# Performance work log

Measured on AMD Instinct MI355X. Metric: run time of the kernel, lower is better.

## Reference

```python
import jax, jax.numpy as jnp
import numpy as np

B, S, D_MODEL, H = 2, 2048, 1024, 16
HD = D_MODEL // H  # 64


def rotate_half(x):
    # pairs (x_even, x_odd) -> (-x_odd, x_even), interleaved back
    x1 = x[..., ::2]
    x2 = x[..., 1::2]
    return jnp.stack([-x2, x1], axis=-1).reshape(x.shape)


def rope_sin_cos(seq_len, head_dim):
    pos = jnp.arange(seq_len, dtype=jnp.float32)
    dim = jnp.arange(head_dim, dtype=jnp.float32)
    theta = 10000.0 ** (-2.0 * jnp.floor(dim / 2.0) / head_dim)
    angles = pos[:, None] * theta[None, :]  # [S, HD]
    return jnp.sin(angles), jnp.cos(angles)


def setup_inputs():
    key = jax.random.key(0)
    ks = jax.random.split(key, 6)
    w_scale = 1.0 / np.sqrt(D_MODEL)
    x = jax.random.normal(ks[0], (B, S, D_MODEL), jnp.float32)
    # causal mask: 1.0 where attention is disallowed (j > i)
    mask = (1.0 - jnp.tril(jnp.ones((S, S), jnp.float32)))[None, None, :, :]
    wq = jax.random.normal(ks[1], (D_MODEL, D_MODEL), jnp.float32) * w_scale
    wk = jax.random.normal(ks[2], (D_MODEL, D_MODEL), jnp.float32) * w_scale
    wv = jax.random.normal(ks[3], (D_MODEL, D_MODEL), jnp.float32) * w_scale
    wo = jax.random.normal(ks[4], (D_MODEL, D_MODEL), jnp.float32) * w_scale
    zeros = jnp.zeros((D_MODEL,), jnp.float32)
    return dict(x=x, mask=mask, wq=wq, bq=zeros, wk=wk, bk=zeros,
                wv=wv, bv=zeros, wo=wo, bo=zeros)


def reference(x, mask, wq, bq, wk, bk, wv, bv, wo, bo):
    b, s, _ = x.shape

    def split_heads(t):  # [B,S,D] -> [B,H,S,HD]
        return t.reshape(b, s, H, HD).transpose(0, 2, 1, 3)

    q = split_heads(x @ wq + bq)
    k = split_heads(x @ wk + bk)
    v = split_heads(x @ wv + bv)

    sin, cos = rope_sin_cos(s, HD)
    sin = sin[None, None, :, :]
    cos = cos[None, None, :, :]
    q = q * cos + rotate_half(q) * sin
    k = k * cos + rotate_half(k) * sin

    logits = jnp.einsum('bhqd,bhkd->bhqk', q, k) / jnp.sqrt(jnp.float32(HD))
    logits = logits + mask * (-1e9)
    attn = jax.nn.softmax(logits, axis=-1)
    out = jnp.einsum('bhqk,bhkd->bhqd', attn, v)  # [B,H,S,HD]
    out = out.transpose(0, 2, 1, 3).reshape(b, s, D_MODEL)
    return out @ wo + bo
```

## Files before the change

kernel.cpp:

```cpp
#include <hip/hip_runtime.h>
#include <hip/hip_bf16.h>


#define S_ 2048
#define DM 1024
#define HD 64

typedef __attribute__((ext_vector_type(8))) short short8;
typedef __attribute__((ext_vector_type(4))) float floatx4;

__device__ __forceinline__ unsigned short f2b(float x) {
  union { __hip_bfloat16 h; unsigned short u; } cv;
  cv.h = __float2bfloat16(x);
  return cv.u;
}

__device__ __forceinline__ void gload_lds16(const unsigned short* g, unsigned short* l) {
  typedef const __attribute__((address_space(1))) unsigned int* gp_t;
  typedef __attribute__((address_space(3))) unsigned int* lp_t;
  __builtin_amdgcn_global_load_lds((gp_t)(const void*)g, (lp_t)(void*)l, 16, 0, 0);
}

__global__ void prep_kernel(const float* __restrict__ x,
                            const float* __restrict__ w0, const float* __restrict__ w1,
                            const float* __restrict__ w2, const float* __restrict__ w3,
                            unsigned short* __restrict__ xc,
                            unsigned short* __restrict__ wt,
                            float2* __restrict__ rope) {
  const int bid = blockIdx.x;
  if (bid < 4096) {
    int i = (bid * 256 + threadIdx.x) * 4;
    float4 v = *(const float4*)(x + i);
    ushort4 o;
    o.x = f2b(v.x); o.y = f2b(v.y); o.z = f2b(v.z); o.w = f2b(v.w);
    *(ushort4*)(xc + i) = o;
  } else if (bid < 8192) {
    __shared__ float tile[32][33];
    const int rem = bid - 4096;
    const int z = rem >> 10;
    const int bx = (rem & 1023) & 31;
    const int by = (rem & 1023) >> 5;
    const float* W = (z == 0) ? w0 : (z == 1) ? w1 : (z == 2) ? w2 : w3;
    unsigned short* Wt = wt + (size_t)z * DM * DM;
    const int tx = threadIdx.x & 31;
    const int ty = threadIdx.x >> 5;
    const int k0 = bx * 32;
    const int c0 = by * 32;
#pragma unroll
    for (int i = 0; i < 4; ++i)
      tile[ty + i * 8][tx] = W[(size_t)(k0 + ty + i * 8) * DM + c0 + tx];
    __syncthreads();
#pragma unroll
    for (int i = 0; i < 4; ++i)
      Wt[(size_t)(c0 + ty + i * 8) * DM + k0 + tx] = f2b(tile[tx][ty + i * 8]);
  } else {
    int i = (bid - 8192) * 256 + threadIdx.x;
    int s = i >> 5, d2 = i & 31;
    float th = expf(-(float)d2 * (9.210340371976184f / 32.0f));
    float sn, cs;
    sincosf((float)s * th, &sn, &cs);
    rope[i] = make_float2(cs, sn);
  }
}

__global__ __launch_bounds__(256, 3) void gemm_qkv(
    const unsigned short* __restrict__ A, const unsigned short* __restrict__ Wt,
    const float* __restrict__ bq, const float* __restrict__ bk,
    const float* __restrict__ bv, const float2* __restrict__ rope,
    unsigned short* __restrict__ QKV) {
  __shared__ __attribute__((aligned(16))) unsigned short As[128 * 64];
  __shared__ __attribute__((aligned(16))) unsigned short Bs[128 * 64];
  const int r0 = blockIdx.x * 128;
  const int c0 = blockIdx.y * 128;
  const int t = threadIdx.x;
  const int lane = t & 63;
  const int wv = t >> 6;
  const int wr = (wv >> 1) * 64;
  const int wc = (wv & 1) * 64;
  const int lr = lane & 15;
  const int lg = lane >> 4;

  const int srow = wv * 32 + (lane >> 3);
  const int sseg = ((lane & 7) ^ (lane >> 3)) * 8;
  const unsigned short* Ag = A + (size_t)(r0 + srow) * DM + sseg;
  const unsigned short* Bg = Wt + (size_t)(c0 + srow) * DM + sseg;
  unsigned short* lA = &As[wv * 32 * 64];
  unsigned short* lB = &Bs[wv * 32 * 64];

  floatx4 acc[4][4] = {};
  const int fswz = (lr & 7) << 4;

  for (int k0 = 0; k0 < DM; k0 += 64) {
#pragma unroll
    for (int j = 0; j < 4; ++j) {
      gload_lds16(Ag + k0 + j * 8 * DM, lA + j * 8 * 64);
      gload_lds16(Bg + k0 + j * 8 * DM, lB + j * 8 * 64);
    }
    __syncthreads();
#pragma unroll
    for (int kk = 0; kk < 2; ++kk) {
      short8 af[4], bf[4];
#pragma unroll
      for (int m = 0; m < 4; ++m)
        af[m] = *(const short8*)((char*)As + (wr + m * 16 + lr) * 128 +
                                 ((kk * 64 + lg * 16) ^ fswz));
#pragma unroll
      for (int n = 0; n < 4; ++n)
        bf[n] = *(const short8*)((char*)Bs + (wc + n * 16 + lr) * 128 +
                                 ((kk * 64 + lg * 16) ^ fswz));
#pragma unroll
      for (int m = 0; m < 4; ++m)
#pragma unroll
        for (int n = 0; n < 4; ++n)
          acc[m][n] = __builtin_amdgcn_mfma_f32_16x16x32_bf16(af[m], bf[n], acc[m][n], 0, 0, 0);
    }
    __syncthreads();
  }

  const int mat = blockIdx.y >> 3;
  const float* bias = (mat == 0) ? bq : (mat == 1) ? bk : bv;
  const int rbase = r0 + wr + lg * 4;
  const int cbase = c0 + wc + lr;
#pragma unroll
  for (int n = 0; n < 4; ++n) {
    const int c = cbase + n * 16;
    const int cc = c & (DM - 1);
    const float bvv = bias[cc];
    const int d = c & 63;
    const int h = cc >> 6;
#pragma unroll
    for (int m = 0; m < 4; ++m) {
#pragma unroll
      for (int i = 0; i < 4; ++i) {
        const int r = rbase + m * 16 + i;
        const int s = r & (S_ - 1);
        const int b = r >> 11;
        float v = acc[m][n][i] + bvv;
        float pv = __shfl_xor(v, 1);
        if (mat < 2) {
          float2 cssn = rope[s * 32 + (d >> 1)];
          v = (d & 1) ? fmaf(v, cssn.x, pv * cssn.y) : fmaf(v, cssn.x, -pv * cssn.y);
          if (mat == 0) v *= 0.18033688011112042f;
        }
        QKV[((size_t)((mat << 5) | (b << 4) | h) * S_ + s) * HD + d] = f2b(v);
      }
    }
  }
}

__global__ __launch_bounds__(256, 3) void gemm_out(
    const unsigned short* __restrict__ A, const unsigned short* __restrict__ Wt,
    const float* __restrict__ bias, float* __restrict__ out) {
  __shared__ __attribute__((aligned(16))) unsigned short As[128 * 64];
  __shared__ __attribute__((aligned(16))) unsigned short Bs[128 * 64];
  const int r0 = blockIdx.x * 128;
  const int c0 = blockIdx.y * 128;
  const int t = threadIdx.x;
  const int lane = t & 63;
  const int wv = t >> 6;
  const int wr = (wv >> 1) * 64;
  const int wc = (wv & 1) * 64;
  const int lr = lane & 15;
  const int lg = lane >> 4;

  const int srow = wv * 32 + (lane >> 3);
  const int sseg = ((lane & 7) ^ (lane >> 3)) * 8;
  const unsigned short* Ag = A + (size_t)(r0 + srow) * DM + sseg;
  const unsigned short* Bg = Wt + (size_t)(c0 + srow) * DM + sseg;
  unsigned short* lA = &As[wv * 32 * 64];
  unsigned short* lB = &Bs[wv * 32 * 64];

  floatx4 acc[4][4] = {};
  const int fswz = (lr & 7) << 4;

  for (int k0 = 0; k0 < DM; k0 += 64) {
#pragma unroll
    for (int j = 0; j < 4; ++j) {
      gload_lds16(Ag + k0 + j * 8 * DM, lA + j * 8 * 64);
      gload_lds16(Bg + k0 + j * 8 * DM, lB + j * 8 * 64);
    }
    __syncthreads();
#pragma unroll
    for (int kk = 0; kk < 2; ++kk) {
      short8 af[4], bf[4];
#pragma unroll
      for (int m = 0; m < 4; ++m)
        af[m] = *(const short8*)((char*)As + (wr + m * 16 + lr) * 128 +
                                 ((kk * 64 + lg * 16) ^ fswz));
#pragma unroll
      for (int n = 0; n < 4; ++n)
        bf[n] = *(const short8*)((char*)Bs + (wc + n * 16 + lr) * 128 +
                                 ((kk * 64 + lg * 16) ^ fswz));
#pragma unroll
      for (int m = 0; m < 4; ++m)
#pragma unroll
        for (int n = 0; n < 4; ++n)
          acc[m][n] = __builtin_amdgcn_mfma_f32_16x16x32_bf16(af[m], bf[n], acc[m][n], 0, 0, 0);
    }
    __syncthreads();
  }

  const int rbase = r0 + wr + lg * 4;
  const int cbase = c0 + wc + lr;
#pragma unroll
  for (int n = 0; n < 4; ++n) {
    const int c = cbase + n * 16;
    const float bvv = bias[c];
#pragma unroll
    for (int m = 0; m < 4; ++m) {
#pragma unroll
      for (int i = 0; i < 4; ++i) {
        const int r = rbase + m * 16 + i;
        out[(size_t)r * DM + c] = acc[m][n][i] + bvv;
      }
    }
  }
}

__global__ __launch_bounds__(256, 4) void attn_kernel(
    const unsigned short* __restrict__ Q, const unsigned short* __restrict__ K,
    const unsigned short* __restrict__ V, unsigned short* __restrict__ AttnC) {
  __shared__ __attribute__((aligned(16))) unsigned short Ks[2][64 * 64];
  __shared__ __attribute__((aligned(16))) unsigned short Vs[2][64 * 64];
  __shared__ __attribute__((aligned(16))) unsigned short Ps[4][16 * 64];

  const int bh = blockIdx.x;
  const int y = (int)blockIdx.y;
  const int ya = y >> 3, yb = y & 7;
  const int qt = (ya & 1) ? (8 * ya + 7 - yb) : (8 * ya + yb);
  const int tid = threadIdx.x;
  const int w = tid >> 6;
  const int l = tid & 63;
  const int lg = l >> 4;
  const int lr = l & 15;
  const size_t base = (size_t)bh * S_ * HD;
  const int qin = w * 16 + lr;

  short8 qf[2];
  {
    const unsigned short* Qrow =
        Q + base + (size_t)(qt * 64 + w * 16 + lr) * HD + lg * 8;
    qf[0] = *(const short8*)(Qrow);
    qf[1] = *(const short8*)(Qrow + 32);
  }

  floatx4 o[4] = {};
  float m = -1e30f, lsum = 0.f;

  const int krow = tid >> 3;
  const int kseg = tid & 7;
  const int oct = tid >> 5;
  const int kp = tid & 31;

  int4 kr0, kr1; short8 va, vb;
  {
    const unsigned short* Kg = K + base;
    const unsigned short* Vg = V + base;
    kr0 = *(const int4*)(Kg + krow * 64 + kseg * 8);
    kr1 = *(const int4*)(Kg + (krow + 32) * 64 + kseg * 8);
    va = *(const short8*)(Vg + (2 * kp) * 64 + oct * 8);
    vb = *(const short8*)(Vg + (2 * kp + 1) * 64 + oct * 8);
  }

  char* const Pw = (char*)Ps[w];
  const int pswz = (lr & 7) << 4;

  for (int t = 0; t <= qt; ++t) {
    const int cur = t & 1;
    {
      char* Kb = (char*)Ks[cur];
      *(int4*)(Kb + krow * 128 + ((kseg * 16) ^ ((krow & 7) << 4))) = kr0;
      *(int4*)(Kb + (krow + 32) * 128 + ((kseg * 16) ^ ((krow & 7) << 4))) = kr1;
      char* Vb = (char*)Vs[cur];
#pragma unroll
      for (int j = 0; j < 8; ++j) {
        int d = oct * 8 + j;
        unsigned int pk = (unsigned int)(unsigned short)va[j] |
                          ((unsigned int)(unsigned short)vb[j] << 16);
        *(unsigned int*)(Vb + d * 128 + ((4 * kp) ^ (j << 4))) = pk;
      }
    }
    if (t < qt) {
      const unsigned short* Kg = K + base + (size_t)(t + 1) * 64 * HD;
      const unsigned short* Vg = V + base + (size_t)(t + 1) * 64 * HD;
      kr0 = *(const int4*)(Kg + krow * 64 + kseg * 8);
      kr1 = *(const int4*)(Kg + (krow + 32) * 64 + kseg * 8);
      va = *(const short8*)(Vg + (2 * kp) * 64 + oct * 8);
      vb = *(const short8*)(Vg + (2 * kp + 1) * 64 + oct * 8);
    }
    __syncthreads();

    floatx4 s[4] = {};
    __builtin_amdgcn_s_setprio(1);
#pragma unroll
    for (int kk = 0; kk < 2; ++kk) {
#pragma unroll
      for (int n = 0; n < 4; ++n) {
        int r = n * 16 + lr;
        short8 kf = *(const short8*)((char*)Ks[cur] + r * 128 +
                                     ((kk * 64 + lg * 16) ^ ((r & 7) << 4)));
        s[n] = __builtin_amdgcn_mfma_f32_16x16x32_bf16(kf, qf[kk], s[n], 0, 0, 0);
      }
    }
    __builtin_amdgcn_s_setprio(0);
    if (t == qt) {
#pragma unroll
      for (int n = 0; n < 4; ++n)
#pragma unroll
        for (int i = 0; i < 4; ++i)
          if (n * 16 + lg * 4 + i > qin) s[n][i] = -1e30f;
    }

    float tm0 = fmaxf(fmaxf(s[0][0], s[0][1]), fmaxf(s[0][2], s[0][3]));
    float tm1 = fmaxf(fmaxf(s[1][0], s[1][1]), fmaxf(s[1][2], s[1][3]));
    float tm2 = fmaxf(fmaxf(s[2][0], s[2][1]), fmaxf(s[2][2], s[2][3]));
    float tm3 = fmaxf(fmaxf(s[3][0], s[3][1]), fmaxf(s[3][2], s[3][3]));
    float tm = fmaxf(fmaxf(tm0, tm1), fmaxf(tm2, tm3));
    tm = fmaxf(tm, __shfl_xor(tm, 16));
    tm = fmaxf(tm, __shfl_xor(tm, 32));
    if (__any(tm > m + 8.f)) {
      const float mn = fmaxf(m, tm);
      const float al = exp2f(m - mn);
      m = mn;
      lsum *= al;
#pragma unroll
      for (int dd = 0; dd < 4; ++dd) o[dd] *= al;
    }
    float ps = 0.f;
#pragma unroll
    for (int n = 0; n < 4; ++n) {
#pragma unroll
      for (int i = 0; i < 4; ++i) {
        float p = exp2f(s[n][i] - m);
        s[n][i] = p;
        ps += p;
      }
    }
    lsum += ps;

#pragma unroll
    for (int n = 0; n < 4; ++n) {
#pragma unroll
      for (int h = 0; h < 2; ++h) {
        unsigned int pk = (unsigned int)f2b(s[n][2 * h]) |
                          ((unsigned int)f2b(s[n][2 * h + 1]) << 16);
        *(unsigned int*)(Pw + lr * 128 + (((n * 16 + lg * 4 + 2 * h) * 2) ^ pswz)) = pk;
      }
    }
    short8 pb[2];
#pragma unroll
    for (int kk = 0; kk < 2; ++kk)
      pb[kk] = *(const short8*)(Pw + lr * 128 + ((kk * 64 + lg * 16) ^ pswz));
    __builtin_amdgcn_s_setprio(1);
#pragma unroll
    for (int kk = 0; kk < 2; ++kk)
#pragma unroll
      for (int dd = 0; dd < 4; ++dd) {
        int d = dd * 16 + lr;
        short8 vbf = *(const short8*)((char*)Vs[cur] + d * 128 +
                                      ((kk * 64 + lg * 16) ^ ((d & 7) << 4)));
        o[dd] = __builtin_amdgcn_mfma_f32_16x16x32_bf16(vbf, pb[kk], o[dd], 0, 0, 0);
      }
    __builtin_amdgcn_s_setprio(0);
  }

  lsum += __shfl_xor(lsum, 16);
  lsum += __shfl_xor(lsum, 32);
  const float inv = 1.f / lsum;
  unsigned short* orow =
      AttnC + (size_t)((bh >> 4) * S_ + qt * 64 + w * 16 + lr) * DM + (bh & 15) * HD;
#pragma unroll
  for (int dd = 0; dd < 4; ++dd) {
    unsigned int w0 = (unsigned int)f2b(o[dd][0] * inv) |
                      ((unsigned int)f2b(o[dd][1] * inv) << 16);
    unsigned int w1 = (unsigned int)f2b(o[dd][2] * inv) |
                      ((unsigned int)f2b(o[dd][3] * inv) << 16);
    *(uint2*)(orow + dd * 16 + lg * 4) = make_uint2(w0, w1);
  }
}

extern "C" void kernel_launch(void* const* d_in, const int* in_sizes, int n_in,
                              void* d_out, int out_size, void* d_ws, size_t ws_size,
                              hipStream_t stream) {
  const float* x = (const float*)d_in[0];
  const float* wq = (const float*)d_in[2];
  const float* bq = (const float*)d_in[3];
  const float* wk = (const float*)d_in[4];
  const float* bk = (const float*)d_in[5];
  const float* wv = (const float*)d_in[6];
  const float* bv = (const float*)d_in[7];
  const float* wo = (const float*)d_in[8];
  const float* bo = (const float*)d_in[9];

  char* ws = (char*)d_ws;
  const size_t MB = 1024ull * 1024ull;
  unsigned short* Xc = (unsigned short*)(ws);
  unsigned short* Wt = (unsigned short*)(ws + 8 * MB);
  unsigned short* QKVb = (unsigned short*)(ws + 16 * MB);
  unsigned short* Ac = (unsigned short*)(ws + 40 * MB);
  float2* rope = (float2*)(ws + 48 * MB);

  prep_kernel<<<8448, 256, 0, stream>>>(x, wq, wk, wv, wo, Xc, Wt, rope);
  gemm_qkv<<<dim3(32, 24), 256, 0, stream>>>(Xc, Wt, bq, bk, bv, rope, QKVb);
  attn_kernel<<<dim3(32, 32), 256, 0, stream>>>(
      QKVb, QKVb + 32ull * S_ * HD, QKVb + 64ull * S_ * HD, Ac);
  gemm_out<<<dim3(32, 8), 256, 0, stream>>>(Ac, Wt + 3ull * DM * DM, bo, (float*)d_out);
}
```

Measured before the change: 118.6 us.

## Stream K tiles directly into LDS with async global_load_lds and unroll by two

K tiles are now prefetched straight into shared memory with global_load_lds, so they no longer pass through registers. The address is pre-swizzled, and explicit vmcnt/lgkmcnt waits plus a raw barrier replace __syncthreads. The loop is unrolled by two so the double-buffer indices become constants, V packing uses v_perm, and the max reduction is reshaped. Query-tile scheduling changes from a zigzag order to a simple reverse order, which puts the heaviest tiles first. The hand-placed wait counts risk races if the compiler reorders memory operations, and the simpler tile order may change load balance.

```diff
diff --git a/kernel.cpp b/kernel.cpp
--- a/kernel.cpp
+++ b/kernel.cpp
@@ -217,6 +217,102 @@
   }
 }
 
+#define ATTN_STEP(TT, BUF, KLA, KLB)                                           \
+  do {                                                                         \
+    {                  \
+      char* Vb = (char*)Vs[BUF];                                               \
+      const unsigned* ua = (const unsigned*)&va;                               \
+      const unsigned* ub = (const unsigned*)&vb;                               \
+      _Pragma("unroll") for (int j = 0; j < 8; ++j) {                          \
+        unsigned pk = __builtin_amdgcn_perm(                                   \
+            ub[j >> 1], ua[j >> 1], (j & 1) ? 0x07060302u : 0x05040100u);      \
+        *(unsigned*)(Vb + (oct * 8 + j) * 128 + ((4 * kp) ^ (j << 4))) = pk;   \
+      }                                                                        \
+    }                                                                          \
+    if ((TT) < qt) {                                \
+      va = *(const short8*)(Vpref);                                            \
+      vb = *(const short8*)(Vpref + 64);                                       \
+      Vpref += 4096;                                                           \
+    }                                                                          \
+                        \
+    asm volatile("s_waitcnt lgkmcnt(0)" ::: "memory");                         \
+    __builtin_amdgcn_s_barrier();                                              \
+                 \
+    if ((TT) < qt) asm volatile("s_waitcnt vmcnt(2)" ::: "memory");            \
+    else           asm volatile("s_waitcnt vmcnt(0)" ::: "memory");            \
+    __builtin_amdgcn_sched_barrier(0);                                         \
+    if ((TT) < qt) {                   \
+      gload_lds16(Kpref, KLA);                                                 \
+      gload_lds16(Kpref + 2048, KLB);                                          \
+      Kpref += 4096;                                                           \
+    }                                                                          \
+                     \
+    floatx4 s[4] = {};                                                         \
+    __builtin_amdgcn_s_setprio(1);                                             \
+    _Pragma("unroll") for (int kk = 0; kk < 2; ++kk) {                         \
+      _Pragma("unroll") for (int n = 0; n < 4; ++n) {                          \
+        int r = n * 16 + lr;                                                   \
+        short8 kf = *(const short8*)((char*)Ks[BUF] + r * 128 +                \
+                                     ((kk * 64 + lg * 16) ^ ((r & 7) << 4)));  \
+        s[n] = __builtin_amdgcn_mfma_f32_16x16x32_bf16(kf, qf[kk], s[n], 0, 0, 0); \
+      }                                                                        \
+    }                                                                          \
+    __builtin_amdgcn_s_setprio(0);                                             \
+    if ((TT) == qt) {                                                          \
+      _Pragma("unroll") for (int n = 0; n < 4; ++n)                            \
+        _Pragma("unroll") for (int i = 0; i < 4; ++i)                          \
+          if (n * 16 + lg * 4 + i > qin) s[n][i] = -1e30f;                     \
+    }                                                                          \
+                                \
+    float ta = fmaxf(fmaxf(s[0][0], s[0][1]), s[0][2]);                        \
+    float tb = fmaxf(fmaxf(s[0][3], s[1][0]), s[1][1]);                        \
+    float tc = fmaxf(fmaxf(s[1][2], s[1][3]), s[2][0]);                        \
+    float td = fmaxf(fmaxf(s[2][1], s[2][2]), s[2][3]);                        \
+    float te = fmaxf(fmaxf(s[3][0], s[3][1]), s[3][2]);                        \
+    float tm = fmaxf(fmaxf(ta, tb), tc);                                       \
+    tm = fmaxf(fmaxf(tm, td), te);                                             \
+    tm = fmaxf(tm, s[3][3]);                                                   \
+    tm = fmaxf(tm, __shfl_xor(tm, 16));                                        \
+    tm = fmaxf(tm, __shfl_xor(tm, 32));                                        \
+    if (__any(tm > m + 8.f)) {                          \
+      const float mn = fmaxf(m, tm);                                           \
+      const float al = exp2f(m - mn);                                          \
+      m = mn;                                                                  \
+      lsum *= al;                                                              \
+      _Pragma("unroll") for (int dd = 0; dd < 4; ++dd) o[dd] *= al;            \
+    }                                                                          \
+    float ps = 0.f;                                                            \
+    _Pragma("unroll") for (int n = 0; n < 4; ++n) {                            \
+      _Pragma("unroll") for (int i = 0; i < 4; ++i) {                          \
+        float p = exp2f(s[n][i] - m);                                          \
+        s[n][i] = p;                                                           \
+        ps += p;                                                               \
+      }                                                                        \
+    }                                                                          \
+    lsum += ps;                                                                \
+                    \
+    _Pragma("unroll") for (int n = 0; n < 4; ++n) {                            \
+      _Pragma("unroll") for (int hh = 0; hh < 2; ++hh) {                       \
+        unsigned pk = (unsigned)f2b(s[n][2 * hh]) |                            \
+                      ((unsigned)f2b(s[n][2 * hh + 1]) << 16);                 \
+        *(unsigned*)(Pw + lr * 128 +                                           \
+                     (((n * 16 + lg * 4 + 2 * hh) * 2) ^ pswz)) = pk;          \
+      }                                                                        \
+    }                                                                          \
+    short8 pb[2];                                                              \
+    _Pragma("unroll") for (int kk = 0; kk < 2; ++kk)                           \
+      pb[kk] = *(const short8*)(Pw + lr * 128 + ((kk * 64 + lg * 16) ^ pswz)); \
+    __builtin_amdgcn_s_setprio(1);                                             \
+    _Pragma("unroll") for (int kk = 0; kk < 2; ++kk)                           \
+      _Pragma("unroll") for (int dd = 0; dd < 4; ++dd) {                       \
+        int d = dd * 16 + lr;                                                  \
+        short8 vbf = *(const short8*)((char*)Vs[BUF] + d * 128 +               \
+                                      ((kk * 64 + lg * 16) ^ ((d & 7) << 4))); \
+        o[dd] = __builtin_amdgcn_mfma_f32_16x16x32_bf16(vbf, pb[kk], o[dd], 0, 0, 0); \
+      }                                                                        \
+    __builtin_amdgcn_s_setprio(0);                                             \
+  } while (0)
+
 __global__ __launch_bounds__(256, 4) void attn_kernel(
     const unsigned short* __restrict__ Q, const unsigned short* __restrict__ K,
     const unsigned short* __restrict__ V, unsigned short* __restrict__ AttnC) {
@@ -225,9 +321,7 @@
   __shared__ __attribute__((aligned(16))) unsigned short Ps[4][16 * 64];
 
   const int bh = blockIdx.x;
-  const int y = (int)blockIdx.y;
-  const int ya = y >> 3, yb = y & 7;
-  const int qt = (ya & 1) ? (8 * ya + 7 - yb) : (8 * ya + yb);
+  const int qt = 31 - (int)blockIdx.y;
   const int tid = threadIdx.x;
   const int w = tid >> 6;
   const int l = tid & 63;
@@ -249,120 +343,33 @@
 
   const int krow = tid >> 3;
   const int kseg = tid & 7;
+  const unsigned short* Kpref = K + base + krow * 64 + ((kseg ^ (krow & 7)) * 8);
+  unsigned short* const kld0a = &Ks[0][w * 512];
+  unsigned short* const kld0b = &Ks[0][2048 + w * 512];
+  unsigned short* const kld1a = &Ks[1][w * 512];
+  unsigned short* const kld1b = &Ks[1][2048 + w * 512];
+
   const int oct = tid >> 5;
   const int kp = tid & 31;
-
-  int4 kr0, kr1; short8 va, vb;
-  {
-    const unsigned short* Kg = K + base;
-    const unsigned short* Vg = V + base;
-    kr0 = *(const int4*)(Kg + krow * 64 + kseg * 8);
-    kr1 = *(const int4*)(Kg + (krow + 32) * 64 + kseg * 8);
-    va = *(const short8*)(Vg + (2 * kp) * 64 + oct * 8);
-    vb = *(const short8*)(Vg + (2 * kp + 1) * 64 + oct * 8);
-  }
+  const unsigned short* Vpref = V + base + 2 * kp * 64 + oct * 8;
+
+  short8 va = *(const short8*)(Vpref);
+  short8 vb = *(const short8*)(Vpref + 64);
+  Vpref += 4096;
+  gload_lds16(Kpref, kld0a);
+  gload_lds16(Kpref + 2048, kld0b);
+  Kpref += 4096;
 
   char* const Pw = (char*)Ps[w];
   const int pswz = (lr & 7) << 4;
 
-  for (int t = 0; t <= qt; ++t) {
-    const int cur = t & 1;
-    {
-      char* Kb = (char*)Ks[cur];
-      *(int4*)(Kb + krow * 128 + ((kseg * 16) ^ ((krow & 7) << 4))) = kr0;
-      *(int4*)(Kb + (krow + 32) * 128 + ((kseg * 16) ^ ((krow & 7) << 4))) = kr1;
-      char* Vb = (char*)Vs[cur];
-#pragma unroll
-      for (int j = 0; j < 8; ++j) {
-        int d = oct * 8 + j;
-        unsigned int pk = (unsigned int)(unsigned short)va[j] |
-                          ((unsigned int)(unsigned short)vb[j] << 16);
-        *(unsigned int*)(Vb + d * 128 + ((4 * kp) ^ (j << 4))) = pk;
-      }
-    }
-    if (t < qt) {
-      const unsigned short* Kg = K + base + (size_t)(t + 1) * 64 * HD;
-      const unsigned short* Vg = V + base + (size_t)(t + 1) * 64 * HD;
-      kr0 = *(const int4*)(Kg + krow * 64 + kseg * 8);
-      kr1 = *(const int4*)(Kg + (krow + 32) * 64 + kseg * 8);
-      va = *(const short8*)(Vg + (2 * kp) * 64 + oct * 8);
-      vb = *(const short8*)(Vg + (2 * kp + 1) * 64 + oct * 8);
-    }
-    __syncthreads();
-
-    floatx4 s[4] = {};
-    __builtin_amdgcn_s_setprio(1);
-#pragma unroll
-    for (int kk = 0; kk < 2; ++kk) {
-#pragma unroll
-      for (int n = 0; n < 4; ++n) {
-        int r = n * 16 + lr;
-        short8 kf = *(const short8*)((char*)Ks[cur] + r * 128 +
-                                     ((kk * 64 + lg * 16) ^ ((r & 7) << 4)));
-        s[n] = __builtin_amdgcn_mfma_f32_16x16x32_bf16(kf, qf[kk], s[n], 0, 0, 0);
-      }
-    }
-    __builtin_amdgcn_s_setprio(0);
-    if (t == qt) {
-#pragma unroll
-      for (int n = 0; n < 4; ++n)
-#pragma unroll
-        for (int i = 0; i < 4; ++i)
-          if (n * 16 + lg * 4 + i > qin) s[n][i] = -1e30f;
-    }
-
-    float tm0 = fmaxf(fmaxf(s[0][0], s[0][1]), fmaxf(s[0][2], s[0][3]));
-    float tm1 = fmaxf(fmaxf(s[1][0], s[1][1]), fmaxf(s[1][2], s[1][3]));
-    float tm2 = fmaxf(fmaxf(s[2][0], s[2][1]), fmaxf(s[2][2], s[2][3]));
-    float tm3 = fmaxf(fmaxf(s[3][0], s[3][1]), fmaxf(s[3][2], s[3][3]));
-    float tm = fmaxf(fmaxf(tm0, tm1), fmaxf(tm2, tm3));
-    tm = fmaxf(tm, __shfl_xor(tm, 16));
-    tm = fmaxf(tm, __shfl_xor(tm, 32));
-    if (__any(tm > m + 8.f)) {
-      const float mn = fmaxf(m, tm);
-      const float al = exp2f(m - mn);
-      m = mn;
-      lsum *= al;
-#pragma unroll
-      for (int dd = 0; dd < 4; ++dd) o[dd] *= al;
-    }
-    float ps = 0.f;
-#pragma unroll
-    for (int n = 0; n < 4; ++n) {
-#pragma unroll
-      for (int i = 0; i < 4; ++i) {
-        float p = exp2f(s[n][i] - m);
-        s[n][i] = p;
-        ps += p;
-      }
-    }
-    lsum += ps;
-
-#pragma unroll
-    for (int n = 0; n < 4; ++n) {
-#pragma unroll
-      for (int h = 0; h < 2; ++h) {
-        unsigned int pk = (unsigned int)f2b(s[n][2 * h]) |
-                          ((unsigned int)f2b(s[n][2 * h + 1]) << 16);
-        *(unsigned int*)(Pw + lr * 128 + (((n * 16 + lg * 4 + 2 * h) * 2) ^ pswz)) = pk;
-      }
-    }
-    short8 pb[2];
-#pragma unroll
-    for (int kk = 0; kk < 2; ++kk)
-      pb[kk] = *(const short8*)(Pw + lr * 128 + ((kk * 64 + lg * 16) ^ pswz));
-    __builtin_amdgcn_s_setprio(1);
-#pragma unroll
-    for (int kk = 0; kk < 2; ++kk)
-#pragma unroll
-      for (int dd = 0; dd < 4; ++dd) {
-        int d = dd * 16 + lr;
-        short8 vbf = *(const short8*)((char*)Vs[cur] + d * 128 +
-                                      ((kk * 64 + lg * 16) ^ ((d & 7) << 4)));
-        o[dd] = __builtin_amdgcn_mfma_f32_16x16x32_bf16(vbf, pb[kk], o[dd], 0, 0, 0);
-      }
-    __builtin_amdgcn_s_setprio(0);
-  }
+  int t = 0;
+#pragma unroll 1
+  for (; t + 1 <= qt; t += 2) {
+    ATTN_STEP(t, 0, kld1a, kld1b);
+    ATTN_STEP(t + 1, 1, kld0a, kld0b);
+  }
+  if (t <= qt) ATTN_STEP(t, 0, kld1a, kld1b);
 
   lsum += __shfl_xor(lsum, 16);
   lsum += __shfl_xor(lsum, 32);
```

Measured after the change: 114.3 us. 1.04x faster.
